# Performance work log

Hardware: AMD Instinct MI355X
Metric: run time of the kernel (lower is better)

Reference implementation:

```python
import jax, jax.numpy as jnp
import numpy as np

# ROIAlign config (torchvision semantics, aligned=False)
SPATIAL_SCALE = 0.25
POOLED = 7
SAMPLING_RATIO = 2
MODE = "max"  # from __init__ mode='max'


def setup_inputs() -> dict:
    key = jax.random.key(0)
    kf, kcx, kcy, kw, kh, kb = jax.random.split(key, 6)
    B, C, H, W = 2, 256, 200, 304
    N = 512
    IMG_H, IMG_W = H / SPATIAL_SCALE, W / SPATIAL_SCALE
    feature = jax.random.normal(kf, (B, C, H, W), dtype=jnp.float32)
    cx = jax.random.uniform(kcx, (N,)) * IMG_W
    cy = jax.random.uniform(kcy, (N,)) * IMG_H
    bw = jax.random.uniform(kw, (N,)) * 192.0 + 16.0
    bh = jax.random.uniform(kh, (N,)) * 192.0 + 16.0
    x1 = jnp.clip(cx - bw * 0.5, 0.0, IMG_W - 2.0)
    y1 = jnp.clip(cy - bh * 0.5, 0.0, IMG_H - 2.0)
    x2 = jnp.clip(cx + bw * 0.5, x1 + 1.0, IMG_W - 1.0)
    y2 = jnp.clip(cy + bh * 0.5, y1 + 1.0, IMG_H - 1.0)
    boxes = jnp.stack([x1, y1, x2, y2], axis=1).astype(jnp.float32)
    batch_idx = jax.random.randint(kb, (N,), 0, B, dtype=jnp.int32)
    return {"feature": feature, "boxes": boxes, "batch_idx": batch_idx}


def _sample_coords(start, size):
    # start,size: [N]; returns [N, POOLED*SAMPLING_RATIO] sample coordinates
    bin_sz = size / POOLED                         # [N]
    p = jnp.arange(POOLED, dtype=jnp.float32)      # bin index
    s = (jnp.arange(SAMPLING_RATIO, dtype=jnp.float32) + 0.5) / SAMPLING_RATIO
    # coord = start + (p + s) * bin_sz  -> [N, POOLED, RATIO]
    c = start[:, None, None] + (p[None, :, None] + s[None, None, :]) * bin_sz[:, None, None]
    return c.reshape(c.shape[0], POOLED * SAMPLING_RATIO)


def roi_align(feature, boxes, batch_idx):
    B, C, H, W = feature.shape
    roi = boxes * SPATIAL_SCALE                    # [N,4] in feature coords
    rs_x, rs_y, re_x, re_y = roi[:, 0], roi[:, 1], roi[:, 2], roi[:, 3]
    roi_w = jnp.maximum(re_x - rs_x, 1.0)
    roi_h = jnp.maximum(re_y - rs_y, 1.0)
    ys = _sample_coords(rs_y, roi_h)               # [N, Sy]
    xs = _sample_coords(rs_x, roi_w)               # [N, Sx]
    y = jnp.broadcast_to(ys[:, :, None], (ys.shape[0], ys.shape[1], xs.shape[1]))
    x = jnp.broadcast_to(xs[:, None, :], y.shape)  # [N, Sy, Sx]

    valid = (y > -1.0) & (y < H) & (x > -1.0) & (x < W)
    y = jnp.clip(y, 0.0, H - 1)
    x = jnp.clip(x, 0.0, W - 1)
    y0 = jnp.floor(y).astype(jnp.int32)
    x0 = jnp.floor(x).astype(jnp.int32)
    y1 = jnp.minimum(y0 + 1, H - 1)
    x1 = jnp.minimum(x0 + 1, W - 1)
    ly = y - y0.astype(y.dtype)
    lx = x - x0.astype(x.dtype)
    hy, hx = 1.0 - ly, 1.0 - lx
    b = batch_idx[:, None, None]
    # advanced indexing -> [N, Sy, Sx, C]
    val = (hy * hx)[..., None] * feature[b, :, y0, x0] \
        + (hy * lx)[..., None] * feature[b, :, y0, x1] \
        + (ly * hx)[..., None] * feature[b, :, y1, x0] \
        + (ly * lx)[..., None] * feature[b, :, y1, x1]
    val = jnp.where(valid[..., None], val, 0.0)
    N = boxes.shape[0]
    val = val.reshape(N, POOLED, SAMPLING_RATIO, POOLED, SAMPLING_RATIO, C)
    if MODE == "max":
        out = val.max(axis=(2, 4))                 # [N, PH, PW, C]
    else:
        out = val.mean(axis=(2, 4))
    return jnp.transpose(out, (0, 3, 1, 2))        # [N, C, PH, PW]


def reference(feature, boxes, batch_idx):
    return roi_align(feature, boxes, batch_idx)
```

## Files before the change

kernel.cpp:

```cpp
#include <hip/hip_runtime.h>


#define SPATIAL_SCALE 0.25f
#define POOLED 7
#define SR 2

constexpr int Bc = 2;
constexpr int Cc = 256;
constexpr int Hc = 200;
constexpr int Wc = 304;
constexpr int Nc = 512;
constexpr int CELLS = POOLED * POOLED;
constexpr int PER_BOX = Cc * CELLS;
constexpr int CHUNKS = PER_BOX / 256;

__global__ __launch_bounds__(256) void roi_align_max_kernel(
    const float* __restrict__ feature,
    const float* __restrict__ boxes,
    const int*   __restrict__ batch_idx,
    float*       __restrict__ out)
{
    int raw   = blockIdx.x;
    int chunk = raw / Nc;
    int n     = raw - chunk * Nc;
    int idx   = n * PER_BOX + chunk * 256 + threadIdx.x;

    int rem = idx - n * PER_BOX;
    int pw  = rem % POOLED;
    int ph  = (rem / POOLED) % POOLED;
    int c   = rem / CELLS;

    float rsx = boxes[n * 4 + 0] * SPATIAL_SCALE;
    float rsy = boxes[n * 4 + 1] * SPATIAL_SCALE;
    float rex = boxes[n * 4 + 2] * SPATIAL_SCALE;
    float rey = boxes[n * 4 + 3] * SPATIAL_SCALE;
    float roi_w = fmaxf(rex - rsx, 1.0f);
    float roi_h = fmaxf(rey - rsy, 1.0f);
    float bin_w = roi_w / (float)POOLED;
    float bin_h = roi_h / (float)POOLED;

    int b = batch_idx[n];
    const float* __restrict__ fptr =
        feature + ((size_t)b * Cc + c) * (size_t)(Hc * Wc);

    int   y0i[SR], y1i[SR], x0i[SR], x1i[SR];
    float ly[SR], hy[SR], lx[SR], hx[SR];
    bool  vy[SR], vx[SR];

    #pragma unroll
    for (int s = 0; s < SR; ++s) {
        float sval = ((float)s + 0.5f) / (float)SR;
        float py = (float)ph + sval;
        float y  = __fadd_rn(rsy, __fmul_rn(py, bin_h));
        vy[s] = (y > -1.0f) && (y < (float)Hc);
        float yc = fminf(fmaxf(y, 0.0f), (float)(Hc - 1));
        int yf = (int)floorf(yc);
        y0i[s] = yf;
        y1i[s] = min(yf + 1, Hc - 1);
        ly[s]  = yc - (float)yf;
        hy[s]  = 1.0f - ly[s];

        float px = (float)pw + sval;
        float x  = __fadd_rn(rsx, __fmul_rn(px, bin_w));
        vx[s] = (x > -1.0f) && (x < (float)Wc);
        float xc = fminf(fmaxf(x, 0.0f), (float)(Wc - 1));
        int xf = (int)floorf(xc);
        x0i[s] = xf;
        x1i[s] = min(xf + 1, Wc - 1);
        lx[s]  = xc - (float)xf;
        hx[s]  = 1.0f - lx[s];
    }

    float m = -INFINITY;
    #pragma unroll
    for (int sy = 0; sy < SR; ++sy) {
        int r0 = y0i[sy] * Wc;
        int r1 = y1i[sy] * Wc;
        #pragma unroll
        for (int sx = 0; sx < SR; ++sx) {
            float v00 = fptr[r0 + x0i[sx]];
            float v01 = fptr[r0 + x1i[sx]];
            float v10 = fptr[r1 + x0i[sx]];
            float v11 = fptr[r1 + x1i[sx]];
            float bil = hy[sy] * hx[sx] * v00 + hy[sy] * lx[sx] * v01 +
                        ly[sy] * hx[sx] * v10 + ly[sy] * lx[sx] * v11;
            float v = (vy[sy] && vx[sx]) ? bil : 0.0f;
            m = fmaxf(m, v);
        }
    }

    out[idx] = m;
}

extern "C" void kernel_launch(void* const* d_in, const int* in_sizes, int n_in,
                              void* d_out, int out_size, void* d_ws, size_t ws_size,
                              hipStream_t stream) {
    const float* feature   = (const float*)d_in[0];
    const float* boxes     = (const float*)d_in[1];
    const int*   batch_idx = (const int*)d_in[2];
    float*       out       = (float*)d_out;

    int grid  = Nc * CHUNKS;
    roi_align_max_kernel<<<grid, 256, 0, stream>>>(feature, boxes, batch_idx, out);
}
```

Measured before the change: 261.4 us.

## Stage ROI sample rows into LDS with float4 loads before bilinear max

Result: faster. 227.8 us (-12.9%).

```diff
diff --git a/kernel.cpp b/kernel.cpp
--- a/kernel.cpp
+++ b/kernel.cpp
@@ -10,9 +10,17 @@
 constexpr int Hc = 200;
 constexpr int Wc = 304;
 constexpr int Nc = 512;
-constexpr int CELLS = POOLED * POOLED;
+
+constexpr int CG      = 4;
+constexpr int NSAMP   = POOLED * SR;
+constexpr int NROW    = NSAMP * 2;
+constexpr int XW      = 64;
+constexpr int XPAD    = 68;
+constexpr int CH_STR  = NROW * XPAD;
+constexpr int CELLS   = POOLED * POOLED;
+constexpr int OUTS    = CG * CELLS;
 constexpr int PER_BOX = Cc * CELLS;
-constexpr int CHUNKS = PER_BOX / 256;
+constexpr int PLANE   = Hc * Wc;
 
 __global__ __launch_bounds__(256) void roi_align_max_kernel(
     const float* __restrict__ feature,
@@ -20,15 +28,12 @@
     const int*   __restrict__ batch_idx,
     float*       __restrict__ out)
 {
-    int raw   = blockIdx.x;
-    int chunk = raw / Nc;
-    int n     = raw - chunk * Nc;
-    int idx   = n * PER_BOX + chunk * 256 + threadIdx.x;
+    __shared__ float lds[CG * CH_STR];
 
-    int rem = idx - n * PER_BOX;
-    int pw  = rem % POOLED;
-    int ph  = (rem / POOLED) % POOLED;
-    int c   = rem / CELLS;
+    int bid = blockIdx.x;
+    int cg  = bid / Nc;
+    int n   = bid - cg * Nc;
+    int tid = threadIdx.x;
 
     float rsx = boxes[n * 4 + 0] * SPATIAL_SCALE;
     float rsy = boxes[n * 4 + 1] * SPATIAL_SCALE;
@@ -38,58 +43,84 @@
     float roi_h = fmaxf(rey - rsy, 1.0f);
     float bin_w = roi_w / (float)POOLED;
     float bin_h = roi_h / (float)POOLED;
+    int b = batch_idx[n];
 
-    int b = batch_idx[n];
-    const float* __restrict__ fptr =
-        feature + ((size_t)b * Cc + c) * (size_t)(Hc * Wc);
+    float x_first = __fadd_rn(rsx, __fmul_rn(0.25f, bin_w));
+    float xc0 = fminf(fmaxf(x_first, 0.0f), (float)(Wc - 1));
+    int xbase = ((int)floorf(xc0)) & ~3;
 
-    int   y0i[SR], y1i[SR], x0i[SR], x1i[SR];
-    float ly[SR], hy[SR], lx[SR], hx[SR];
-    bool  vy[SR], vx[SR];
+    const float* __restrict__ gbase =
+        feature + ((size_t)b * Cc + (size_t)cg * CG) * (size_t)PLANE;
 
+    int lane16 = tid & 15;
+    int rbase  = tid >> 4;
     #pragma unroll
-    for (int s = 0; s < SR; ++s) {
-        float sval = ((float)s + 0.5f) / (float)SR;
-        float py = (float)ph + sval;
-        float y  = __fadd_rn(rsy, __fmul_rn(py, bin_h));
-        vy[s] = (y > -1.0f) && (y < (float)Hc);
-        float yc = fminf(fmaxf(y, 0.0f), (float)(Hc - 1));
-        int yf = (int)floorf(yc);
-        y0i[s] = yf;
-        y1i[s] = min(yf + 1, Hc - 1);
-        ly[s]  = yc - (float)yf;
-        hy[s]  = 1.0f - ly[s];
+    for (int it = 0; it < 7; ++it) {
+        int r       = it * 16 + rbase;
+        int c_local = r / NROW;
+        int slot    = r - c_local * NROW;
+        int s       = slot >> 1;
+        int which   = slot & 1;
+        int p       = s >> 1;
+        int sub     = s & 1;
+        float py = (float)p + ((float)sub + 0.5f) * 0.5f;
+        float fy = __fadd_rn(rsy, __fmul_rn(py, bin_h));
+        float fyc = fminf(fmaxf(fy, 0.0f), (float)(Hc - 1));
+        int y0 = (int)floorf(fyc);
+        int row = which ? min(y0 + 1, Hc - 1) : y0;
 
-        float px = (float)pw + sval;
-        float x  = __fadd_rn(rsx, __fmul_rn(px, bin_w));
-        vx[s] = (x > -1.0f) && (x < (float)Wc);
-        float xc = fminf(fmaxf(x, 0.0f), (float)(Wc - 1));
-        int xf = (int)floorf(xc);
-        x0i[s] = xf;
-        x1i[s] = min(xf + 1, Wc - 1);
-        lx[s]  = xc - (float)xf;
-        hx[s]  = 1.0f - lx[s];
+        int col = xbase + lane16 * 4;
+        col = min(col, Wc - 4);
+        const float4 v = *(const float4*)(gbase + (size_t)c_local * PLANE
+                                          + row * Wc + col);
+        *(float4*)&lds[c_local * CH_STR + slot * XPAD + lane16 * 4] = v;
     }
+    __syncthreads();
 
-    float m = -INFINITY;
-    #pragma unroll
-    for (int sy = 0; sy < SR; ++sy) {
-        int r0 = y0i[sy] * Wc;
-        int r1 = y1i[sy] * Wc;
+    if (tid < OUTS) {
+        int c_local = tid / CELLS;
+        int cell    = tid - c_local * CELLS;
+        int ph      = cell / POOLED;
+        int pw      = cell - ph * POOLED;
+        const float* __restrict__ L = &lds[c_local * CH_STR];
+
+        float m = -INFINITY;
         #pragma unroll
-        for (int sx = 0; sx < SR; ++sx) {
-            float v00 = fptr[r0 + x0i[sx]];
-            float v01 = fptr[r0 + x1i[sx]];
-            float v10 = fptr[r1 + x0i[sx]];
-            float v11 = fptr[r1 + x1i[sx]];
-            float bil = hy[sy] * hx[sx] * v00 + hy[sy] * lx[sx] * v01 +
-                        ly[sy] * hx[sx] * v10 + ly[sy] * lx[sx] * v11;
-            float v = (vy[sy] && vx[sx]) ? bil : 0.0f;
-            m = fmaxf(m, v);
+        for (int sy = 0; sy < SR; ++sy) {
+            int sY = ph * SR + sy;
+            float py = (float)ph + ((float)sy + 0.5f) * 0.5f;
+            float fy = __fadd_rn(rsy, __fmul_rn(py, bin_h));
+            bool vy = (fy > -1.0f) && (fy < (float)Hc);
+            float fyc = fminf(fmaxf(fy, 0.0f), (float)(Hc - 1));
+            int y0 = (int)floorf(fyc);
+            float ly = fyc - (float)y0;
+            float hy = 1.0f - ly;
+            const float* __restrict__ r0 = L + (2 * sY) * XPAD;
+            const float* __restrict__ r1 = L + (2 * sY + 1) * XPAD;
+
+            #pragma unroll
+            for (int sx = 0; sx < SR; ++sx) {
+                float px = (float)pw + ((float)sx + 0.5f) * 0.5f;
+                float fx = __fadd_rn(rsx, __fmul_rn(px, bin_w));
+                bool vx = (fx > -1.0f) && (fx < (float)Wc);
+                float fxc = fminf(fmaxf(fx, 0.0f), (float)(Wc - 1));
+                int x0 = (int)floorf(fxc);
+                float lx = fxc - (float)x0;
+                float hx = 1.0f - lx;
+                int c0 = x0 - xbase;
+                int x1 = min(x0 + 1, Wc - 1);
+                int c1 = x1 - xbase;
+
+                float v00 = r0[c0], v01 = r0[c1];
+                float v10 = r1[c0], v11 = r1[c1];
+                float bil = hy * hx * v00 + hy * lx * v01 +
+                            ly * hx * v10 + ly * lx * v11;
+                float v = (vy && vx) ? bil : 0.0f;
+                m = fmaxf(m, v);
+            }
         }
+        out[(size_t)n * PER_BOX + cg * OUTS + tid] = m;
     }
-
-    out[idx] = m;
 }
 
 extern "C" void kernel_launch(void* const* d_in, const int* in_sizes, int n_in,
@@ -100,6 +131,6 @@
     const int*   batch_idx = (const int*)d_in[2];
     float*       out       = (float*)d_out;
 
-    int grid  = Nc * CHUNKS;
+    int grid = (Cc / CG) * Nc;
     roi_align_max_kernel<<<grid, 256, 0, stream>>>(feature, boxes, batch_idx, out);
 }
```
